# Kernel optimization log

Measured on AMD Instinct MI355X. Metric: run time of the kernel, lower is better.

The kernel has to match this reference:

```python
import jax, jax.numpy as jnp
import numpy as np

A, B, O, ACT, H, NH = 16, 8192, 128, 16, 128, 4
D = H // NH  # attend_dim
IN = O + ACT
NEG = -1e9


def setup_inputs() -> dict:
    key = jax.random.key(0)
    ks = jax.random.split(key, 16)
    s = lambda k, shape, fan: jax.random.normal(k, shape, jnp.float32) / np.sqrt(fan)
    return {
        "obs": jax.random.normal(ks[0], (A, B, O), jnp.float32),
        "actions": jax.random.uniform(ks[1], (A, B, ACT), jnp.float32),
        # per-agent sa-encoder (enc_fc1)
        "W_sa": s(ks[2], (A, IN, H), IN), "b_sa": jnp.zeros((A, H), jnp.float32),
        # per-agent state encoder (s_enc_fc1)
        "W_s": s(ks[3], (A, O, H), O), "b_s": jnp.zeros((A, H), jnp.float32),
        # shared per-head extractors
        "Wk": s(ks[4], (NH, H, D), H),
        "Wsel": s(ks[5], (NH, H, D), H),
        "Wv": s(ks[6], (NH, H, D), H), "bv": jnp.zeros((NH, D), jnp.float32),
        # per-agent critic MLP
        "Wc1": s(ks[7], (A, 2 * H, H), 2 * H), "bc1": jnp.zeros((A, H), jnp.float32),
        "Wc2": s(ks[8], (A, H, ACT), H), "bc2": jnp.zeros((A, ACT), jnp.float32),
    }


def _bn(x):
    # BatchNorm1d(affine=False) in training mode: normalize over batch axis, biased var
    m = x.mean(axis=1, keepdims=True)
    v = x.var(axis=1, keepdims=True)
    return (x - m) / jnp.sqrt(v + 1e-5)


def reference(obs, actions, W_sa, b_sa, W_s, b_s, Wk, Wsel, Wv, bv, Wc1, bc1, Wc2, bc2):
    lrelu = jax.nn.leaky_relu  # slope 0.01, matches torch default
    inp = jnp.concatenate([obs, actions], axis=-1)            # [A,B,IN]
    sa = lrelu(jnp.einsum('abi,aih->abh', _bn(inp), W_sa) + b_sa[:, None, :])  # [A,B,H]
    se = lrelu(jnp.einsum('abo,aoh->abh', _bn(obs), W_s) + b_s[:, None, :])    # [A,B,H]
    keys = jnp.einsum('abh,nhd->nabd', sa, Wk)                # [NH,A,B,D]
    vals = lrelu(jnp.einsum('abh,nhd->nabd', sa, Wv) + bv[:, None, None, :])
    sel = jnp.einsum('abh,nhd->nabd', se, Wsel)
    logits = jnp.einsum('nibd,njbd->nibj', sel, keys) / np.sqrt(D)  # [NH,A,B,A]
    self_mask = jnp.eye(A, dtype=bool)[None, :, None, :]      # mask j == i
    w = jax.nn.softmax(jnp.where(self_mask, NEG, logits), axis=-1)
    other = jnp.einsum('nibj,njbd->nibd', w, vals)            # [NH,A,B,D]
    other = jnp.transpose(other, (1, 2, 0, 3)).reshape(A, B, NH * D)  # head-order concat
    cin = jnp.concatenate([se, other], axis=-1)               # [A,B,2H]
    h = lrelu(jnp.einsum('abk,akh->abh', cin, Wc1) + bc1[:, None, :])
    all_q = jnp.einsum('abh,aho->abo', h, Wc2) + bc2[:, None, :]      # [A,B,ACT]
    idx = jnp.argmax(actions, axis=-1)[..., None]             # int_acs, [A,B,1]
    q = jnp.take_along_axis(all_q, idx, axis=-1)              # [A,B,1]
    return q
```

## Files before the change

### kernel.cpp

```cpp
#include <hip/hip_runtime.h>
#include <hip/hip_bf16.h>

#define A_N 16
#define B_N 8192
#define O_N 128
#define ACT_N 16
#define H_N 128
#define NH_N 4
#define D_N 32
#define IN_N 144
#define NEGV -1e9f

typedef __attribute__((ext_vector_type(8))) short short8;
typedef __attribute__((ext_vector_type(4))) float floatx4;

static __device__ inline unsigned short f2bf(float f) {
    union { float f; unsigned u; } x{f};
    unsigned u = x.u + 0x7FFFu + ((x.u >> 16) & 1u);
    return (unsigned short)(u >> 16);
}
static __device__ inline unsigned pack_bf2(float a, float b) {
    union { float f; unsigned u; } xa{a}, xb{b};
    unsigned ua = xa.u + 0x7FFFu + ((xa.u >> 16) & 1u);
    unsigned ub = xb.u + 0x7FFFu + ((xb.u >> 16) & 1u);
    return (ua >> 16) | (ub & 0xFFFF0000u);
}
static __device__ inline float bf2f(unsigned short h) {
    union { unsigned u; float f; } x;
    x.u = ((unsigned)h) << 16;
    return x.f;
}
static __device__ inline float bflo(unsigned u) {
    union { unsigned u; float f; } x; x.u = u << 16; return x.f;
}
static __device__ inline float bfhi(unsigned u) {
    union { unsigned u; float f; } x; x.u = u & 0xFFFF0000u; return x.f;
}
static __device__ inline short8 ld_frag(const unsigned* p) {
    union { unsigned u[4]; short8 v; } x;
    uint2 lo = *(const uint2*)p;
    uint2 hi = *(const uint2*)(p + 2);
    x.u[0] = lo.x; x.u[1] = lo.y; x.u[2] = hi.x; x.u[3] = hi.y;
    return x.v;
}
static __device__ inline short8 ld_frag4(const unsigned* p) {
    union { uint4 q; short8 v; } x;
    x.q = *(const uint4*)p;
    return x.v;
}

__global__ __launch_bounds__(256) void k_stats(const float* __restrict__ obs,
                                               const float* __restrict__ act,
                                               float* __restrict__ gsumP,
                                               float* __restrict__ gsqP) {
    __shared__ float ssum[IN_N];
    __shared__ float ssq[IN_N];
    int a = blockIdx.x >> 4;
    int slab = blockIdx.x & 15;
    int r0 = slab * 512;
    int t = threadIdx.x;
    if (t < IN_N) { ssum[t] = 0.f; ssq[t] = 0.f; }
    __syncthreads();
    {
        int c0 = (t & 31) * 4, rg = t >> 5;
        const float* p = obs + ((size_t)a * B_N + r0 + rg) * O_N + c0;
        float s0 = 0.f, s1 = 0.f, s2 = 0.f, s3 = 0.f;
        float q0 = 0.f, q1 = 0.f, q2 = 0.f, q3 = 0.f;
#pragma unroll 4
        for (int i = 0; i < 64; ++i) {
            float4 v = *(const float4*)(p + (size_t)i * 8 * O_N);
            s0 += v.x; q0 += v.x * v.x;
            s1 += v.y; q1 += v.y * v.y;
            s2 += v.z; q2 += v.z * v.z;
            s3 += v.w; q3 += v.w * v.w;
        }
        atomicAdd(&ssum[c0 + 0], s0); atomicAdd(&ssq[c0 + 0], q0);
        atomicAdd(&ssum[c0 + 1], s1); atomicAdd(&ssq[c0 + 1], q1);
        atomicAdd(&ssum[c0 + 2], s2); atomicAdd(&ssq[c0 + 2], q2);
        atomicAdd(&ssum[c0 + 3], s3); atomicAdd(&ssq[c0 + 3], q3);
    }
    if (t < 128) {
        int f = t & 15, rg = t >> 4;
        const float* p = act + ((size_t)a * B_N + r0 + rg) * ACT_N + f;
        float s = 0.f, q = 0.f;
#pragma unroll 4
        for (int i = 0; i < 64; ++i) {
            float v = p[(size_t)i * 8 * ACT_N];
            s += v; q += v * v;
        }
        atomicAdd(&ssum[O_N + f], s);
        atomicAdd(&ssq[O_N + f], q);
    }
    __syncthreads();
    if (t < IN_N) {
        gsumP[(a * 16 + slab) * IN_N + t] = ssum[t];
        gsqP[(a * 16 + slab) * IN_N + t] = ssq[t];
    }
}

__global__ __launch_bounds__(256) void k_finalize(const float* __restrict__ gsumP,
                                                  const float* __restrict__ gsqP,
                                                  float* __restrict__ mean,
                                                  float* __restrict__ rstd) {
    int i = blockIdx.x * 256 + threadIdx.x;
    if (i < A_N * IN_N) {
        int a = i / IN_N, f = i - a * IN_N;
        float s = 0.f, q = 0.f;
#pragma unroll
        for (int sl = 0; sl < 16; ++sl) {
            s += gsumP[(a * 16 + sl) * IN_N + f];
            q += gsqP[(a * 16 + sl) * IN_N + f];
        }
        const float invB = 1.f / (float)B_N;
        float m = s * invB;
        float v = fmaxf(q * invB - m * m, 0.f);
        mean[i] = m;
        rstd[i] = rsqrtf(v + 1e-5f);
    }
}

#define L1E 393216
#define P1E 409600
#define P2E 417792
#define CRE 679936
#define C2E 712704
#define BFE (C2E + 4096)
__global__ __launch_bounds__(256) void k_wprep(
    const float* __restrict__ W_sa, const float* __restrict__ W_s,
    const float* __restrict__ Wk, const float* __restrict__ Wsel,
    const float* __restrict__ Wv, const float* __restrict__ Wc1,
    const float* __restrict__ Wc2, const float* __restrict__ mean,
    const float* __restrict__ rstd,
    const float* __restrict__ b_sa, const float* __restrict__ b_s,
    unsigned* __restrict__ wt_l1, unsigned* __restrict__ wt_p1,
    unsigned* __restrict__ wt_p2, unsigned* __restrict__ wt_cr,
    float* __restrict__ wt_c2, float* __restrict__ fb) {
    int idx = blockIdx.x * 256 + threadIdx.x;
    if (idx < L1E) {
        int a = idx / 24576, rem = idx % 24576;
        int n = rem & 255, kp = rem >> 8;
        int k0 = 2 * kp, k1 = k0 + 1;
        float v0 = 0.f, v1 = 0.f;
        if (n < 128) {
            if (k0 < IN_N) v0 = W_sa[((size_t)a * IN_N + k0) * H_N + n] * rstd[a * IN_N + k0];
            if (k1 < IN_N) v1 = W_sa[((size_t)a * IN_N + k1) * H_N + n] * rstd[a * IN_N + k1];
        } else {
            int m = n - 128;
            if (k0 < O_N) v0 = W_s[((size_t)a * O_N + k0) * H_N + m] * rstd[a * IN_N + k0];
            if (k1 < O_N) v1 = W_s[((size_t)a * O_N + k1) * H_N + m] * rstd[a * IN_N + k1];
        }
        wt_l1[(size_t)a * 24576 + n * 96 + kp] = pack_bf2(v0, v1);
    } else if (idx < P1E) {
        int i2 = idx - L1E;
        int n = i2 & 255, kp = i2 >> 8;
        int k0 = 2 * kp;
        float v0, v1;
        if (n < 128) {
            const float* w = Wk + ((size_t)(n >> 5) * H_N) * D_N + (n & 31);
            v0 = w[(size_t)k0 * D_N]; v1 = w[(size_t)(k0 + 1) * D_N];
        } else {
            int m = n - 128;
            const float* w = Wv + ((size_t)(m >> 5) * H_N) * D_N + (m & 31);
            v0 = w[(size_t)k0 * D_N]; v1 = w[(size_t)(k0 + 1) * D_N];
        }
        wt_p1[n * 64 + kp] = pack_bf2(v0, v1);
    } else if (idx < P2E) {
        int i3 = idx - P1E;
        int n = i3 & 127, kp = i3 >> 7;
        int k0 = 2 * kp;
        const float* w = Wsel + ((size_t)(n >> 5) * H_N) * D_N + (n & 31);
        wt_p2[n * 64 + kp] = pack_bf2(w[(size_t)k0 * D_N], w[(size_t)(k0 + 1) * D_N]);
    } else if (idx < CRE) {
        int i4 = idx - P2E;
        int a = i4 >> 14, r = i4 & 16383;
        int n = r & 127, kp = r >> 7;
        int k0 = 2 * kp;
        const float* w = Wc1 + (size_t)a * 256 * H_N + n;
        wt_cr[(size_t)a * 16384 + n * 128 + kp] =
            pack_bf2(w[(size_t)k0 * H_N], w[(size_t)(k0 + 1) * H_N]);
    } else if (idx < C2E) {
        int i5 = idx - CRE;
        int a = i5 >> 11, rem = i5 & 2047;
        int oo = rem >> 7, h = rem & 127;
        wt_c2[i5] = Wc2[((size_t)a * H_N + h) * ACT_N + oo];
    } else if (idx < BFE) {
        int i6 = idx - C2E;
        int a = i6 >> 8, c = i6 & 255;
        float s = 0.f;
        if (c < 128) {
            for (int k = 0; k < IN_N; ++k)
                s += mean[a * IN_N + k] * rstd[a * IN_N + k] *
                     W_sa[((size_t)a * IN_N + k) * H_N + c];
            fb[a * 128 + c] = b_sa[a * H_N + c] - s;
        } else {
            int m = c - 128;
            for (int k = 0; k < O_N; ++k)
                s += mean[a * IN_N + k] * rstd[a * IN_N + k] *
                     W_s[((size_t)a * O_N + k) * H_N + m];
            fb[2048 + a * 128 + m] = b_s[a * H_N + m] - s;
        }
    }
}

__global__ __launch_bounds__(512, 2) void k_l1(
    const float* __restrict__ obs, const float* __restrict__ act,
    const unsigned* __restrict__ wt_l1, const float* __restrict__ fb,
    unsigned short* __restrict__ sa_us, unsigned short* __restrict__ se_us,
    int b0g, int Bc) {
    __shared__ unsigned smem[(128 + 256) * 34];
    unsigned* Xs = smem;
    unsigned* Ws = smem + 128 * 34;

    int a = blockIdx.y;
    int b0 = blockIdx.x * 128;
    int t = threadIdx.x;
    int wid = t >> 6, lane = t & 63, lm = lane & 15, lq = lane >> 4;
    int wrow = (wid & 1) * 64;
    int wcol = (wid >> 1) * 64;

    floatx4 acc[4][4];
#pragma unroll
    for (int mt = 0; mt < 4; ++mt)
#pragma unroll
        for (int nt = 0; nt < 4; ++nt)
#pragma unroll
            for (int e = 0; e < 4; ++e) acc[mt][nt][e] = 0.f;

    const unsigned* WtA = wt_l1 + (size_t)a * 24576;

    for (int c = 0; c < 3; ++c) {
        int kk = c * 64;
        __syncthreads();
        for (int idx = t; idx < 128 * 16; idx += 512) {
            int r = idx >> 4, c4 = idx & 15;
            int k = kk + c4 * 4;
            size_t grow = (size_t)a * B_N + b0g + b0 + r;
            float4 v;
            if (k < O_N) v = *(const float4*)&obs[grow * O_N + k];
            else if (k < IN_N) v = *(const float4*)&act[grow * ACT_N + (k - O_N)];
            else v = make_float4(0.f, 0.f, 0.f, 0.f);
            uint2* dst = (uint2*)&Xs[r * 34 + c4 * 2];
            *dst = make_uint2(pack_bf2(v.x, v.y), pack_bf2(v.z, v.w));
        }
        for (int idx = t; idx < 256 * 8; idx += 512) {
            int n = idx >> 3, c4 = idx & 7;
            uint4 w = *(const uint4*)&WtA[(size_t)n * 96 + (kk >> 1) + c4 * 4];
            uint2* dst = (uint2*)&Ws[n * 34 + c4 * 4];
            dst[0] = make_uint2(w.x, w.y);
            dst[1] = make_uint2(w.z, w.w);
        }
        __syncthreads();
#pragma unroll
        for (int s = 0; s < 2; ++s) {
            if (kk + s * 32 >= 160) break;
            short8 afr[4];
#pragma unroll
            for (int mt = 0; mt < 4; ++mt)
                afr[mt] = ld_frag(&Xs[(wrow + mt * 16 + lm) * 34 + s * 16 + lq * 4]);
#pragma unroll
            for (int nt = 0; nt < 4; ++nt) {
                short8 bfr = ld_frag(&Ws[(wcol + nt * 16 + lm) * 34 + s * 16 + lq * 4]);
#pragma unroll
                for (int mt = 0; mt < 4; ++mt)
                    acc[mt][nt] = __builtin_amdgcn_mfma_f32_16x16x32_bf16(
                        afr[mt], bfr, acc[mt][nt], 0, 0, 0);
            }
        }
    }

    int zsel = (wcol >= 128);
    unsigned short* outp = zsel ? se_us : sa_us;
    const float* bias = fb + zsel * 2048 + a * 128;
    int cbase = wcol & 127;
#pragma unroll
    for (int mt = 0; mt < 4; ++mt)
#pragma unroll
        for (int nt = 0; nt < 4; ++nt)
#pragma unroll
            for (int r = 0; r < 4; ++r) {
                int row = wrow + mt * 16 + lq * 4 + r;
                int col = cbase + nt * 16 + lm;
                float v = acc[mt][nt][r] + bias[col];
                v = v > 0.f ? v : 0.01f * v;
                outp[((size_t)(b0 + row) * 16 + a) * 128 + col] = f2bf(v);
            }
}

__global__ __launch_bounds__(256, 3) void k_fused(
    const unsigned* __restrict__ sa_u, const unsigned* __restrict__ se_u,
    const unsigned* __restrict__ wt_p1, const unsigned* __restrict__ wt_p2,
    const float* __restrict__ bv, unsigned short* __restrict__ other_us,
    int Bc) {
    __shared__ unsigned Xs[64 * 66];
    __shared__ unsigned short keys_s[64 * 130];
    __shared__ unsigned short valsT[4 * 128 * 16];
    unsigned short* sel_s = (unsigned short*)Xs;

    int bg0 = blockIdx.x * 4;
    int t = threadIdx.x;
    int wid = t >> 6, lane = t & 63, lm = lane & 15, lq = lane >> 4;

    const unsigned* sa_base = sa_u + (size_t)(bg0 * 16) * 64;
    const unsigned* se_base = se_u + (size_t)(bg0 * 16) * 64;

    for (int idx = t; idx < 64 * 16; idx += 256) {
        int r = idx >> 4, c4 = idx & 15;
        uint4 v = *(const uint4*)&sa_base[(size_t)idx * 4];
        uint2* dst = (uint2*)&Xs[r * 66 + c4 * 4];
        dst[0] = make_uint2(v.x, v.y);
        dst[1] = make_uint2(v.z, v.w);
    }
    uint4 seR[4];
#pragma unroll
    for (int ii = 0; ii < 4; ++ii)
        seR[ii] = *(const uint4*)&se_base[(size_t)(t + ii * 256) * 4];
    __syncthreads();

    {
        floatx4 acc[4][4];
#pragma unroll
        for (int mt = 0; mt < 4; ++mt)
#pragma unroll
            for (int nt = 0; nt < 4; ++nt)
#pragma unroll
                for (int e = 0; e < 4; ++e) acc[mt][nt][e] = 0.f;
#pragma unroll
        for (int s = 0; s < 4; ++s) {
            short8 afr[4];
#pragma unroll
            for (int mt = 0; mt < 4; ++mt)
                afr[mt] = ld_frag(&Xs[(mt * 16 + lm) * 66 + s * 16 + lq * 4]);
#pragma unroll
            for (int nt = 0; nt < 4; ++nt) {
                int col = wid * 64 + nt * 16 + lm;
                short8 bfr = ld_frag4(wt_p1 + (size_t)col * 64 + s * 16 + lq * 4);
#pragma unroll
                for (int mt = 0; mt < 4; ++mt)
                    acc[mt][nt] = __builtin_amdgcn_mfma_f32_16x16x32_bf16(
                        afr[mt], bfr, acc[mt][nt], 0, 0, 0);
            }
        }
        if (wid < 2) {
#pragma unroll
            for (int mt = 0; mt < 4; ++mt)
#pragma unroll
                for (int nt = 0; nt < 4; ++nt)
#pragma unroll
                    for (int r = 0; r < 4; ++r) {
                        int row = mt * 16 + lq * 4 + r;
                        int col = wid * 64 + nt * 16 + lm;
                        keys_s[row * 130 + col] = f2bf(acc[mt][nt][r]);
                    }
        } else {
#pragma unroll
            for (int mt = 0; mt < 4; ++mt)
#pragma unroll
                for (int nt = 0; nt < 4; ++nt) {
                    int d = (wid - 2) * 64 + nt * 16 + lm;
                    float bvc = bv[d];
                    float v0 = acc[mt][nt][0] + bvc; v0 = v0 > 0.f ? v0 : 0.01f * v0;
                    float v1 = acc[mt][nt][1] + bvc; v1 = v1 > 0.f ? v1 : 0.01f * v1;
                    float v2 = acc[mt][nt][2] + bvc; v2 = v2 > 0.f ? v2 : 0.01f * v2;
                    float v3 = acc[mt][nt][3] + bvc; v3 = v3 > 0.f ? v3 : 0.01f * v3;
                    uint2 o = make_uint2(pack_bf2(v0, v1), pack_bf2(v2, v3));
                    *(uint2*)&valsT[mt * 2048 + d * 16 + lq * 4] = o;
                }
        }
    }
    __syncthreads();

#pragma unroll
    for (int ii = 0; ii < 4; ++ii) {
        int idx = t + ii * 256;
        int r = idx >> 4, c4 = idx & 15;
        uint2* dst = (uint2*)&Xs[r * 66 + c4 * 4];
        dst[0] = make_uint2(seR[ii].x, seR[ii].y);
        dst[1] = make_uint2(seR[ii].z, seR[ii].w);
    }
    __syncthreads();

    {
        int wcol = wid * 32;
        floatx4 acc[4][2];
#pragma unroll
        for (int mt = 0; mt < 4; ++mt)
#pragma unroll
            for (int nt = 0; nt < 2; ++nt)
#pragma unroll
                for (int e = 0; e < 4; ++e) acc[mt][nt][e] = 0.f;
#pragma unroll
        for (int s = 0; s < 4; ++s) {
            short8 afr[4];
#pragma unroll
            for (int mt = 0; mt < 4; ++mt)
                afr[mt] = ld_frag(&Xs[(mt * 16 + lm) * 66 + s * 16 + lq * 4]);
#pragma unroll
            for (int nt = 0; nt < 2; ++nt) {
                int col = wcol + nt * 16 + lm;
                short8 bfr = ld_frag4(wt_p2 + (size_t)col * 64 + s * 16 + lq * 4);
#pragma unroll
                for (int mt = 0; mt < 4; ++mt)
                    acc[mt][nt] = __builtin_amdgcn_mfma_f32_16x16x32_bf16(
                        afr[mt], bfr, acc[mt][nt], 0, 0, 0);
            }
        }
        __syncthreads();
#pragma unroll
        for (int mt = 0; mt < 4; ++mt)
#pragma unroll
            for (int nt = 0; nt < 2; ++nt)
#pragma unroll
                for (int r = 0; r < 4; ++r) {
                    int row = mt * 16 + lq * 4 + r;
                    int col = wcol + nt * 16 + lm;
                    sel_s[row * 132 + col] = f2bf(acc[mt][nt][r]);
                }
    }
    __syncthreads();

    const unsigned* selU = (const unsigned*)sel_s;
    const unsigned* keysU = (const unsigned*)keys_s;
    int bsub = wid;
    floatx4 lgacc[4];
#pragma unroll
    for (int n = 0; n < 4; ++n) {
        short8 af = ld_frag(&keysU[(bsub * 16 + lm) * 65 + n * 16 + lq * 4]);
        short8 bf = ld_frag(&selU[(bsub * 16 + lm) * 66 + n * 16 + lq * 4]);
        floatx4 z4 = {0.f, 0.f, 0.f, 0.f};
        lgacc[n] = __builtin_amdgcn_mfma_f32_16x16x32_bf16(af, bf, z4, 0, 0, 0);
    }

    const float scale = 0.17677669529663687f;
    int dr = lm - lq * 4;
    unsigned pq0[4], pq1[4];
#pragma unroll
    for (int n = 0; n < 4; ++n) {
        float p0 = lgacc[n][0] * scale;
        float p1 = lgacc[n][1] * scale;
        float p2 = lgacc[n][2] * scale;
        float p3 = lgacc[n][3] * scale;
        if (dr == 0) p0 = NEGV;
        if (dr == 1) p1 = NEGV;
        if (dr == 2) p2 = NEGV;
        if (dr == 3) p3 = NEGV;
        float m = fmaxf(fmaxf(p0, p1), fmaxf(p2, p3));
        m = fmaxf(m, __shfl_xor(m, 16));
        m = fmaxf(m, __shfl_xor(m, 32));
        p0 = __expf(p0 - m); p1 = __expf(p1 - m);
        p2 = __expf(p2 - m); p3 = __expf(p3 - m);
        float s = p0 + p1 + p2 + p3;
        s += __shfl_xor(s, 16);
        s += __shfl_xor(s, 32);
        float inv = 1.f / s;
        pq0[n] = pack_bf2(p0 * inv, p1 * inv);
        pq1[n] = pack_bf2(p2 * inv, p3 * inv);
    }

    const unsigned* valsTU = (const unsigned*)valsT;
    int g = lq & 1;
    int s0l = (g << 5) + lm;
    int s1l = s0l + 16;
    size_t obase = ((size_t)(bg0 + bsub) * 16 + lm) * 128;
#pragma unroll
    for (int n = 0; n < 4; ++n) {
        unsigned b0 = __shfl(pq0[n], s0l);
        unsigned b1 = __shfl(pq1[n], s0l);
        unsigned b2 = __shfl(pq0[n], s1l);
        unsigned b3 = __shfl(pq1[n], s1l);
        if (lq >= 2) { b0 = 0u; b1 = 0u; b2 = 0u; b3 = 0u; }
        short8 bfr;
        {
            union { unsigned u[4]; short8 v; } x;
            x.u[0] = b0; x.u[1] = b1; x.u[2] = b2; x.u[3] = b3;
            bfr = x.v;
        }
#pragma unroll
        for (int dt = 0; dt < 2; ++dt) {
            int d = n * 32 + dt * 16 + lm;
            uint4 av = *(const uint4*)(valsTU + ((bsub << 10) + d * 8 + (g << 2)));
            if (lq >= 2) { av.x = 0u; av.y = 0u; av.z = 0u; av.w = 0u; }
            short8 afr;
            { union { uint4 q; short8 v; } x; x.q = av; afr = x.v; }
            floatx4 z4 = {0.f, 0.f, 0.f, 0.f};
            floatx4 c = __builtin_amdgcn_mfma_f32_16x16x32_bf16(afr, bfr, z4, 0, 0, 0);
            uint2 o = make_uint2(pack_bf2(c[0], c[1]), pack_bf2(c[2], c[3]));
            *(uint2*)&other_us[obase + n * 32 + dt * 16 + lq * 4] = o;
        }
    }
}

__global__ __launch_bounds__(256, 4) void k_critic(
    const unsigned* __restrict__ se_u, const unsigned* __restrict__ other_u,
    const unsigned* __restrict__ wt_cr,
    const float* __restrict__ bc1, const float* __restrict__ actions,
    const float* __restrict__ wt_c2, const float* __restrict__ bc2,
    float* __restrict__ qout, int b0g, int Bc) {
    __shared__ unsigned smem[(64 + 128) * 34];
    unsigned* Xs = smem;
    unsigned* Ws = smem + 64 * 34;

    int a = blockIdx.y;
    int b0 = blockIdx.x * 64;
    int t = threadIdx.x;
    int wid = t >> 6, lane = t & 63, lm = lane & 15, lq = lane >> 4;
    int wrow = (wid & 1) * 32;
    int wcol = (wid >> 1) * 64;

    floatx4 acc[2][4];
#pragma unroll
    for (int mt = 0; mt < 2; ++mt)
#pragma unroll
        for (int nt = 0; nt < 4; ++nt)
#pragma unroll
            for (int e = 0; e < 4; ++e) acc[mt][nt][e] = 0.f;

    const unsigned* WtA = wt_cr + (size_t)a * 16384;

    for (int c = 0; c < 4; ++c) {
        int kk = c * 64;
        __syncthreads();
        const unsigned* src = (c < 2) ? se_u : other_u;
        int off = (c & 1) * 32;
        for (int idx = t; idx < 64 * 8; idx += 256) {
            int r = idx >> 3, c4 = idx & 7;
            uint4 v = *(const uint4*)&src[((size_t)(b0 + r) * 16 + a) * 64 + off + c4 * 4];
            uint2* dst = (uint2*)&Xs[r * 34 + c4 * 4];
            dst[0] = make_uint2(v.x, v.y);
            dst[1] = make_uint2(v.z, v.w);
        }
        for (int idx = t; idx < 128 * 8; idx += 256) {
            int n = idx >> 3, c4 = idx & 7;
            uint4 w = *(const uint4*)&WtA[(size_t)n * 128 + (kk >> 1) + c4 * 4];
            uint2* dst = (uint2*)&Ws[n * 34 + c4 * 4];
            dst[0] = make_uint2(w.x, w.y);
            dst[1] = make_uint2(w.z, w.w);
        }
        __syncthreads();
#pragma unroll
        for (int s = 0; s < 2; ++s) {
            short8 afr[2];
#pragma unroll
            for (int mt = 0; mt < 2; ++mt)
                afr[mt] = ld_frag(&Xs[(wrow + mt * 16 + lm) * 34 + s * 16 + lq * 4]);
#pragma unroll
            for (int nt = 0; nt < 4; ++nt) {
                short8 bfr = ld_frag(&Ws[(wcol + nt * 16 + lm) * 34 + s * 16 + lq * 4]);
#pragma unroll
                for (int mt = 0; mt < 2; ++mt)
                    acc[mt][nt] = __builtin_amdgcn_mfma_f32_16x16x32_bf16(
                        afr[mt], bfr, acc[mt][nt], 0, 0, 0);
            }
        }
    }

    __syncthreads();
    unsigned short* hbuf = (unsigned short*)smem;
#pragma unroll
    for (int mt = 0; mt < 2; ++mt)
#pragma unroll
        for (int nt = 0; nt < 4; ++nt)
#pragma unroll
            for (int r = 0; r < 4; ++r) {
                int row = wrow + mt * 16 + lq * 4 + r;
                int col = wcol + nt * 16 + lm;
                float v = acc[mt][nt][r] + bc1[a * H_N + col];
                v = v > 0.f ? v : 0.01f * v;
                hbuf[row * 132 + col] = f2bf(v);
            }
    __syncthreads();
    if (t < 64) {
        size_t arow = (size_t)a * B_N + b0g + b0 + t;
        const float* ap = &actions[arow * ACT_N];
        float bestv = ap[0];
        int bi = 0;
        for (int o = 1; o < ACT_N; ++o) {
            float v = ap[o];
            if (v > bestv) { bestv = v; bi = o; }
        }
        float q = bc2[a * ACT_N + bi];
        const float4* w4p = (const float4*)&wt_c2[((size_t)a * ACT_N + bi) * H_N];
        const uint2* hp2 = (const uint2*)&hbuf[t * 132];
#pragma unroll
        for (int h4 = 0; h4 < 32; ++h4) {
            float4 w4 = w4p[h4];
            uint2 hh = hp2[h4];
            q = fmaf(bflo(hh.x), w4.x, q);
            q = fmaf(bfhi(hh.x), w4.y, q);
            q = fmaf(bflo(hh.y), w4.z, q);
            q = fmaf(bfhi(hh.y), w4.w, q);
        }
        qout[arow] = q;
    }
}

extern "C" void kernel_launch(void* const* d_in, const int* in_sizes, int n_in,
                              void* d_out, int out_size, void* d_ws, size_t ws_size,
                              hipStream_t stream) {
    const float* obs     = (const float*)d_in[0];
    const float* actions = (const float*)d_in[1];
    const float* W_sa    = (const float*)d_in[2];
    const float* b_sa    = (const float*)d_in[3];
    const float* W_s     = (const float*)d_in[4];
    const float* b_s     = (const float*)d_in[5];
    const float* Wk      = (const float*)d_in[6];
    const float* Wsel    = (const float*)d_in[7];
    const float* Wv      = (const float*)d_in[8];
    const float* bv      = (const float*)d_in[9];
    const float* Wc1     = (const float*)d_in[10];
    const float* bc1     = (const float*)d_in[11];
    const float* Wc2     = (const float*)d_in[12];
    const float* bc2     = (const float*)d_in[13];
    float* out = (float*)d_out;
    char* ws = (char*)d_ws;

    size_t o = 0;
    float* gsumP = (float*)(ws + o); o += (size_t)36864 * 4;
    float* gsqP  = (float*)(ws + o); o += (size_t)36864 * 4;
    float* meanA = (float*)(ws + o); o += 2304 * 4;
    float* rstdA = (float*)(ws + o); o += 2304 * 4;
    unsigned* wt_l1 = (unsigned*)(ws + o); o += (size_t)393216 * 4;
    unsigned* wt_p1 = (unsigned*)(ws + o); o += (size_t)16384 * 4;
    unsigned* wt_p2 = (unsigned*)(ws + o); o += (size_t)8192 * 4;
    unsigned* wt_cr = (unsigned*)(ws + o); o += (size_t)262144 * 4;
    float* fb = (float*)(ws + o); o += (size_t)4096 * 4;
    float* wt_c2 = (float*)(ws + o); o += (size_t)32768 * 4;
    size_t fixed = o;

    int Bc = B_N;
    while (Bc > 128 && fixed + 12288ull * Bc > ws_size) Bc >>= 1;

    unsigned short* sa_us = (unsigned short*)(ws + o); o += (size_t)A_N * Bc * 128 * 2;
    unsigned short* se_us = (unsigned short*)(ws + o); o += (size_t)A_N * Bc * 128 * 2;
    unsigned short* ot_us = (unsigned short*)(ws + o); o += (size_t)A_N * Bc * 128 * 2;

    k_stats<<<dim3(A_N * 16), 256, 0, stream>>>(obs, actions, gsumP, gsqP);
    k_finalize<<<dim3(9), 256, 0, stream>>>(gsumP, gsqP, meanA, rstdA);
    k_wprep<<<dim3(BFE / 256), 256, 0, stream>>>(W_sa, W_s, Wk, Wsel, Wv, Wc1, Wc2,
                                                 meanA, rstdA, b_sa, b_s,
                                                 wt_l1, wt_p1, wt_p2, wt_cr, wt_c2, fb);

    for (int b0g = 0; b0g < B_N; b0g += Bc) {
        k_l1<<<dim3(Bc / 128, A_N), 512, 0, stream>>>(
            obs, actions, wt_l1, fb, sa_us, se_us, b0g, Bc);
        k_fused<<<dim3(Bc / 4), 256, 0, stream>>>(
            (const unsigned*)sa_us, (const unsigned*)se_us, wt_p1, wt_p2, bv,
            ot_us, Bc);
        k_critic<<<dim3(Bc / 64, A_N), 256, 0, stream>>>(
            (const unsigned*)se_us, (const unsigned*)ot_us, wt_cr, bc1,
            actions, wt_c2, bc2, out, b0g, Bc);
    }
}
```

Baseline: 266.6 us.

## Keep values in registers and exchange softmax weights via LDS in fused attention

Each wave now computes the key and value columns for its own head, not having two waves do keys and two do values. The value results stay in registers and are redistributed with lane shuffles, which removes the valsT shared buffer. The softmax weights are passed between waves through LDS that reuses the keys buffer, which costs one extra barrier. The smaller LDS footprint lets the launch bound rise from 3 to 4 blocks per SM, aiming for higher occupancy in exchange for more register pressure and extra synchronization.

```diff
diff --git a/kernel.cpp b/kernel.cpp
--- a/kernel.cpp
+++ b/kernel.cpp
@@ -46,6 +46,11 @@
 static __device__ inline short8 ld_frag4(const unsigned* p) {
     union { uint4 q; short8 v; } x;
     x.q = *(const uint4*)p;
+    return x.v;
+}
+static __device__ inline short8 mk_frag(unsigned a, unsigned b, unsigned c, unsigned d) {
+    union { unsigned u[4]; short8 v; } x;
+    x.u[0] = a; x.u[1] = b; x.u[2] = c; x.u[3] = d;
     return x.v;
 }
 
@@ -286,15 +291,15 @@
             }
 }
 
-__global__ __launch_bounds__(256, 3) void k_fused(
+__global__ __launch_bounds__(256, 4) void k_fused(
     const unsigned* __restrict__ sa_u, const unsigned* __restrict__ se_u,
     const unsigned* __restrict__ wt_p1, const unsigned* __restrict__ wt_p2,
     const float* __restrict__ bv, unsigned short* __restrict__ other_us,
     int Bc) {
     __shared__ unsigned Xs[64 * 66];
     __shared__ unsigned short keys_s[64 * 130];
-    __shared__ unsigned short valsT[4 * 128 * 16];
     unsigned short* sel_s = (unsigned short*)Xs;
+    unsigned* P_lds = (unsigned*)keys_s;
 
     int bg0 = blockIdx.x * 4;
     int t = threadIdx.x;
@@ -316,6 +321,7 @@
         seR[ii] = *(const uint4*)&se_base[(size_t)(t + ii * 256) * 4];
     __syncthreads();
 
+    unsigned vp[4][2][2];
     {
         floatx4 acc[4][4];
 #pragma unroll
@@ -332,7 +338,8 @@
                 afr[mt] = ld_frag(&Xs[(mt * 16 + lm) * 66 + s * 16 + lq * 4]);
 #pragma unroll
             for (int nt = 0; nt < 4; ++nt) {
-                int col = wid * 64 + nt * 16 + lm;
+                int col = (nt < 2) ? (wid * 32 + nt * 16 + lm)
+                                   : (128 + wid * 32 + (nt - 2) * 16 + lm);
                 short8 bfr = ld_frag4(wt_p1 + (size_t)col * 64 + s * 16 + lq * 4);
 #pragma unroll
                 for (int mt = 0; mt < 4; ++mt)
@@ -340,32 +347,30 @@
                         afr[mt], bfr, acc[mt][nt], 0, 0, 0);
             }
         }
-        if (wid < 2) {
-#pragma unroll
-            for (int mt = 0; mt < 4; ++mt)
-#pragma unroll
-                for (int nt = 0; nt < 4; ++nt)
-#pragma unroll
-                    for (int r = 0; r < 4; ++r) {
-                        int row = mt * 16 + lq * 4 + r;
-                        int col = wid * 64 + nt * 16 + lm;
-                        keys_s[row * 130 + col] = f2bf(acc[mt][nt][r]);
-                    }
-        } else {
-#pragma unroll
-            for (int mt = 0; mt < 4; ++mt)
-#pragma unroll
-                for (int nt = 0; nt < 4; ++nt) {
-                    int d = (wid - 2) * 64 + nt * 16 + lm;
-                    float bvc = bv[d];
-                    float v0 = acc[mt][nt][0] + bvc; v0 = v0 > 0.f ? v0 : 0.01f * v0;
-                    float v1 = acc[mt][nt][1] + bvc; v1 = v1 > 0.f ? v1 : 0.01f * v1;
-                    float v2 = acc[mt][nt][2] + bvc; v2 = v2 > 0.f ? v2 : 0.01f * v2;
-                    float v3 = acc[mt][nt][3] + bvc; v3 = v3 > 0.f ? v3 : 0.01f * v3;
-                    uint2 o = make_uint2(pack_bf2(v0, v1), pack_bf2(v2, v3));
-                    *(uint2*)&valsT[mt * 2048 + d * 16 + lq * 4] = o;
+#pragma unroll
+        for (int mt = 0; mt < 4; ++mt)
+#pragma unroll
+            for (int nt = 0; nt < 2; ++nt) {
+                int col = wid * 32 + nt * 16 + lm;
+#pragma unroll
+                for (int r = 0; r < 4; ++r) {
+                    int row = mt * 16 + lq * 4 + r;
+                    keys_s[row * 130 + col] = f2bf(acc[mt][nt][r]);
                 }
-        }
+            }
+#pragma unroll
+        for (int mt = 0; mt < 4; ++mt)
+#pragma unroll
+            for (int dt = 0; dt < 2; ++dt) {
+                int d = wid * 32 + dt * 16 + lm;
+                float bvc = bv[d];
+                float v0 = acc[mt][dt + 2][0] + bvc; v0 = v0 > 0.f ? v0 : 0.01f * v0;
+                float v1 = acc[mt][dt + 2][1] + bvc; v1 = v1 > 0.f ? v1 : 0.01f * v1;
+                float v2 = acc[mt][dt + 2][2] + bvc; v2 = v2 > 0.f ? v2 : 0.01f * v2;
+                float v3 = acc[mt][dt + 2][3] + bvc; v3 = v3 > 0.f ? v3 : 0.01f * v3;
+                vp[mt][dt][0] = pack_bf2(v0, v1);
+                vp[mt][dt][1] = pack_bf2(v2, v3);
+            }
     }
     __syncthreads();
 
@@ -420,15 +425,16 @@
 
     const unsigned* selU = (const unsigned*)sel_s;
     const unsigned* keysU = (const unsigned*)keys_s;
-    int bsub = wid;
+    int bsub0 = wid;
     floatx4 lgacc[4];
 #pragma unroll
     for (int n = 0; n < 4; ++n) {
-        short8 af = ld_frag(&keysU[(bsub * 16 + lm) * 65 + n * 16 + lq * 4]);
-        short8 bf = ld_frag(&selU[(bsub * 16 + lm) * 66 + n * 16 + lq * 4]);
+        short8 af = ld_frag(&keysU[(bsub0 * 16 + lm) * 65 + n * 16 + lq * 4]);
+        short8 bf = ld_frag(&selU[(bsub0 * 16 + lm) * 66 + n * 16 + lq * 4]);
         floatx4 z4 = {0.f, 0.f, 0.f, 0.f};
         lgacc[n] = __builtin_amdgcn_mfma_f32_16x16x32_bf16(af, bf, z4, 0, 0, 0);
     }
+    __syncthreads();
 
     const float scale = 0.17677669529663687f;
     int dr = lm - lq * 4;
@@ -455,36 +461,39 @@
         pq0[n] = pack_bf2(p0 * inv, p1 * inv);
         pq1[n] = pack_bf2(p2 * inv, p3 * inv);
     }
-
-    const unsigned* valsTU = (const unsigned*)valsT;
+    {
+        uint2* Pw = (uint2*)P_lds;
+#pragma unroll
+        for (int n = 0; n < 4; ++n)
+            Pw[(wid * 4 + n) * 64 + lane] = make_uint2(pq0[n], pq1[n]);
+    }
+    __syncthreads();
+
+    const uint2* Pp = (const uint2*)P_lds;
     int g = lq & 1;
-    int s0l = (g << 5) + lm;
-    int s1l = s0l + 16;
-    size_t obase = ((size_t)(bg0 + bsub) * 16 + lm) * 128;
-#pragma unroll
-    for (int n = 0; n < 4; ++n) {
-        unsigned b0 = __shfl(pq0[n], s0l);
-        unsigned b1 = __shfl(pq1[n], s0l);
-        unsigned b2 = __shfl(pq0[n], s1l);
-        unsigned b3 = __shfl(pq1[n], s1l);
-        if (lq >= 2) { b0 = 0u; b1 = 0u; b2 = 0u; b3 = 0u; }
-        short8 bfr;
-        {
-            union { unsigned u[4]; short8 v; } x;
-            x.u[0] = b0; x.u[1] = b1; x.u[2] = b2; x.u[3] = b3;
-            bfr = x.v;
-        }
+    int sA0 = g * 32 + lm;
+    int sA1 = g * 32 + 16 + lm;
+    bool kz = (lq >= 2);
+#pragma unroll
+    for (int bsub = 0; bsub < 4; ++bsub) {
+        uint2 pa = Pp[(bsub * 4 + wid) * 64 + sA0];
+        uint2 pb = Pp[(bsub * 4 + wid) * 64 + sA1];
+        unsigned b0 = pa.x, b1 = pa.y, b2 = pb.x, b3 = pb.y;
+        if (kz) { b0 = 0u; b1 = 0u; b2 = 0u; b3 = 0u; }
+        short8 bfr = mk_frag(b0, b1, b2, b3);
 #pragma unroll
         for (int dt = 0; dt < 2; ++dt) {
-            int d = n * 32 + dt * 16 + lm;
-            uint4 av = *(const uint4*)(valsTU + ((bsub << 10) + d * 8 + (g << 2)));
-            if (lq >= 2) { av.x = 0u; av.y = 0u; av.z = 0u; av.w = 0u; }
-            short8 afr;
-            { union { uint4 q; short8 v; } x; x.q = av; afr = x.v; }
+            unsigned a0 = __shfl(vp[bsub][dt][0], sA0);
+            unsigned a1 = __shfl(vp[bsub][dt][1], sA0);
+            unsigned a2 = __shfl(vp[bsub][dt][0], sA1);
+            unsigned a3 = __shfl(vp[bsub][dt][1], sA1);
+            if (kz) { a0 = 0u; a1 = 0u; a2 = 0u; a3 = 0u; }
+            short8 afr = mk_frag(a0, a1, a2, a3);
             floatx4 z4 = {0.f, 0.f, 0.f, 0.f};
             floatx4 c = __builtin_amdgcn_mfma_f32_16x16x32_bf16(afr, bfr, z4, 0, 0, 0);
             uint2 o = make_uint2(pack_bf2(c[0], c[1]), pack_bf2(c[2], c[3]));
-            *(uint2*)&other_us[obase + n * 32 + dt * 16 + lq * 4] = o;
+            *(uint2*)&other_us[((size_t)(bg0 + bsub) * 16 + lm) * 128 +
+                               wid * 32 + dt * 16 + lq * 4] = o;
         }
     }
 }
```

Result: slower. 277.3 us (+4.0%).
